# Kernel tuning notes

Measured on AMD Instinct MI355X. Metric: run time of the kernel, lower is better.

## Reference

```python
import jax, jax.numpy as jnp
import numpy as np

HEADS = 4
KNN = 32
N_KEYS = 512
K_DIM = 512
HALF = K_DIM // 2
V_DIM = 1024
IN_DIM = 1024


def setup_inputs() -> dict:
    key = jax.random.key(0)
    k1, k2, k3, k4, k5 = jax.random.split(key, 5)
    x = jax.random.normal(k1, (1, 2048, IN_DIM), dtype=jnp.float32)
    w_q = jax.random.normal(k2, (HEADS * K_DIM, IN_DIM), dtype=jnp.float32) * (IN_DIM ** -0.5)
    b_q = jax.random.normal(k3, (HEADS * K_DIM,), dtype=jnp.float32) * 0.01
    # subkeys: uniform(-1/sqrt(half), 1/sqrt(half)) as in get_uniform_keys
    bound = 1.0 / np.sqrt(HALF)
    keys = jax.random.uniform(k4, (HEADS, 2, N_KEYS, HALF), dtype=jnp.float32,
                              minval=-bound, maxval=bound)
    # values: normal(0, v_dim**-0.5)
    values = jax.random.normal(k5, (N_KEYS * N_KEYS, V_DIM), dtype=jnp.float32) * (V_DIM ** -0.5)
    return {"x": x, "w_q": w_q, "b_q": b_q, "keys": keys, "values": values}


def reference(x, w_q, b_q, keys, values):
    B, S, D = x.shape
    bs = B * S
    # query projection: (bs, heads*k_dim) -> (bs, heads, 2, half)
    q = (x.reshape(bs, D) @ w_q.T + b_q).reshape(bs, HEADS, 2, HALF)
    # per-head, per-half subkey scores: (bs, heads, 2, n_keys)
    scores = jnp.einsum('bhtd,htnd->bhtn', q, keys)
    s_top, i_top = jax.lax.top_k(scores, KNN)          # (bs, heads, 2, knn)
    s1, s2 = s_top[:, :, 0], s_top[:, :, 1]
    i1, i2 = i_top[:, :, 0], i_top[:, :, 1]
    # cross-product of the two half top-k sets: (bs, heads, knn*knn)
    all_s = (s1[..., :, None] + s2[..., None, :]).reshape(bs, HEADS, KNN * KNN)
    all_i = (i1[..., :, None] * N_KEYS + i2[..., None, :]).reshape(bs, HEADS, KNN * KNN)
    best_s, best_pos = jax.lax.top_k(all_s, KNN)       # (bs, heads, knn)
    idx = jnp.take_along_axis(all_i, best_pos, axis=-1)
    # softmax over knn per head (matches softmax on scores.view(-1, knn))
    w = jax.nn.softmax(best_s, axis=-1).reshape(bs, HEADS * KNN)
    idx = idx.reshape(bs, HEADS * KNN)
    # weighted EmbeddingBag gather-sum over the value table
    out = jnp.einsum('bk,bkd->bd', w, values[idx])     # (bs, v_dim)
    return out.reshape(B, S, V_DIM)
```

## Files before the change

### kernel.cpp

```cpp
#include <hip/hip_runtime.h>
#include <math.h>

#define BSZ   2048
#define INDIM 1024
#define QDIM  2048
#define NHT   8
#define NKEYS 512
#define HALFD 256
#define KNN   32
#define VDIM  1024
#define HEADS 4

typedef _Float16 v8h __attribute__((ext_vector_type(8)));
typedef _Float16 v4h __attribute__((ext_vector_type(4)));
typedef float    v4f __attribute__((ext_vector_type(4)));

template<int KSHIFT, bool ASIDE>
__device__ __forceinline__ void split4(const float* __restrict__ in,
                                       _Float16* __restrict__ out, int i) {
  const long e0 = (long)i * 4;
  const int K = 1 << KSHIFT;
  const long r = e0 >> KSHIFT;
  const int k = (int)(e0 & (K - 1));
  const float4 a = *(const float4*)&in[e0];
  const float av[4] = {a.x, a.y, a.z, a.w};
  v4h hv, dv, mv;
  #pragma unroll
  for (int u = 0; u < 4; ++u) {
    const _Float16 hh = (_Float16)av[u];
    hv[u] = hh;
    mv[u] = (_Float16)((av[u] - (float)hh) * 64.0f);
    dv[u] = (_Float16)((float)hh * 0.015625f);
  }
  _Float16* base = out + r * (3L * K) + k;
  *(v4h*)(base)         = hv;
  *(v4h*)(base + K)     = ASIDE ? dv : mv;
  *(v4h*)(base + 2 * K) = ASIDE ? mv : dv;
}

__global__ __launch_bounds__(256) void split_all_kernel(
    const float* __restrict__ x, const float* __restrict__ wq, const float* __restrict__ ky,
    _Float16* __restrict__ xs, _Float16* __restrict__ wqs, _Float16* __restrict__ kys) {
  const int i = blockIdx.x * 256 + threadIdx.x;
  if (i < 524288)            split4<10, true >(x,  xs,  i);
  else if (i < 1048576)      split4<10, false>(wq, wqs, i - 524288);
  else                       split4<8,  false>(ky, kys, i - 1048576);
}

__device__ __forceinline__ void gload16(const _Float16* g, _Float16* l) {
  __builtin_amdgcn_global_load_lds(
      (const __attribute__((address_space(1))) unsigned int*)g,
      (__attribute__((address_space(3))) unsigned int*)l, 16, 0, 0);
}

template<bool Q_EPI>
__global__ __launch_bounds__(256) void mfma_gemm(
    const _Float16* __restrict__ A, int lda, long aBS,
    const _Float16* __restrict__ B, int ldb, long bBS,
    const float* __restrict__ bias,
    float* __restrict__ Cf, int ldc, long cBS,
    _Float16* __restrict__ Cq, int K) {
  extern __shared__ __align__(16) char smem[];
  _Float16* Asm = (_Float16*)smem;
  _Float16* Bsm = (_Float16*)(smem + 16384);
  const int t = threadIdx.x;
  const int z = blockIdx.z;
  const _Float16* Ab = A + (size_t)z * aBS;
  const _Float16* Bb = B + (size_t)z * bBS;
  const int m0 = blockIdx.y * 128, n0 = blockIdx.x * 128;

  const int o0 = t * 16;
  const int os = o0 ^ (((o0 >> 7) & 3) << 4);
  const int sr = os >> 6;
  const int sk = (os & 63) >> 1;
  const _Float16* gA0 = Ab + (size_t)(m0 + sr) * lda + sk;
  const _Float16* gA1 = Ab + (size_t)(m0 + sr + 64) * lda + sk;
  const _Float16* gB0 = Bb + (size_t)(n0 + sr) * ldb + sk;
  const _Float16* gB1 = Bb + (size_t)(n0 + sr + 64) * ldb + sk;

  const int lane = t & 63, w = t >> 6;
  const int wr = (w >> 1) * 64, wc = (w & 1) * 64;
  const int fr = lane & 15, kg = lane >> 4;

  int aoff[4], boff[4];
  #pragma unroll
  for (int i = 0; i < 4; ++i) {
    const int ra = wr + i * 16 + fr;
    aoff[i] = (ra * 64 + ((kg ^ ((ra >> 1) & 3)) * 16)) >> 1;
    const int rb = wc + i * 16 + fr;
    boff[i] = (rb * 64 + ((kg ^ ((rb >> 1) & 3)) * 16)) >> 1;
  }

  v4f acc[4][4];
  #pragma unroll
  for (int i = 0; i < 4; ++i)
    #pragma unroll
    for (int j = 0; j < 4; ++j)
      acc[i][j] = (v4f){0.f, 0.f, 0.f, 0.f};

  gload16(gA0, Asm + t * 8);
  gload16(gA1, Asm + 2048 + t * 8);
  gload16(gB0, Bsm + t * 8);
  gload16(gB1, Bsm + 2048 + t * 8);
  __syncthreads();

  int cur = 0;
  for (int kt = 0; kt < K; kt += 32) {
    const int nxt = cur ^ 1;
    if (kt + 32 < K) {
      gload16(gA0 + kt + 32, Asm + nxt * 4096 + t * 8);
      gload16(gA1 + kt + 32, Asm + nxt * 4096 + 2048 + t * 8);
      gload16(gB0 + kt + 32, Bsm + nxt * 4096 + t * 8);
      gload16(gB1 + kt + 32, Bsm + nxt * 4096 + 2048 + t * 8);
    }
    v8h af[4], bf[4];
    #pragma unroll
    for (int i = 0; i < 4; ++i) af[i] = *(const v8h*)(Asm + cur * 4096 + aoff[i]);
    #pragma unroll
    for (int j = 0; j < 4; ++j) bf[j] = *(const v8h*)(Bsm + cur * 4096 + boff[j]);
    #pragma unroll
    for (int i = 0; i < 4; ++i)
      #pragma unroll
      for (int j = 0; j < 4; ++j)
        acc[i][j] = __builtin_amdgcn_mfma_f32_16x16x32_f16(af[i], bf[j], acc[i][j], 0, 0, 0);
    __syncthreads();
    cur = nxt;
  }

  if (Q_EPI) {
    float* Ct = (float*)smem;
    #pragma unroll
    for (int half = 0; half < 2; ++half) {
      __syncthreads();
      if ((w & 1) == half) {
        #pragma unroll
        for (int j = 0; j < 4; ++j) {
          const int colq = j * 16 + fr;
          const float bv = bias[n0 + half * 64 + colq];
          #pragma unroll
          for (int i = 0; i < 4; ++i)
            #pragma unroll
            for (int rr = 0; rr < 4; ++rr)
              Ct[(wr + i * 16 + kg * 4 + rr) * 68 + colq] = acc[i][j][rr] + bv;
        }
      }
      __syncthreads();
      const int r = t >> 1, cb = (t & 1) * 32;
      const int gcol = n0 + half * 64 + cb;
      const int ht = gcol >> 8, dd = gcol & 255;
      _Float16* p = Cq + (size_t)(m0 + r) * (3 * HALFD * NHT) + ht * (3 * HALFD) + dd;
      #pragma unroll
      for (int u = 0; u < 32; u += 8) {
        float vv[8];
        *(float4*)&vv[0] = *(const float4*)&Ct[r * 68 + cb + u];
        *(float4*)&vv[4] = *(const float4*)&Ct[r * 68 + cb + u + 4];
        v8h hv, dv, mv;
        #pragma unroll
        for (int e = 0; e < 8; ++e) {
          const _Float16 hh = (_Float16)vv[e];
          hv[e] = hh;
          mv[e] = (_Float16)((vv[e] - (float)hh) * 64.0f);
          dv[e] = (_Float16)((float)hh * 0.015625f);
        }
        *(v8h*)(p + u) = hv;
        *(v8h*)(p + HALFD + u) = dv;
        *(v8h*)(p + 2 * HALFD + u) = mv;
      }
    }
  } else {
    float* Cb = Cf + (size_t)z * cBS;
    #pragma unroll
    for (int i = 0; i < 4; ++i)
      #pragma unroll
      for (int j = 0; j < 4; ++j)
        #pragma unroll
        for (int rr = 0; rr < 4; ++rr) {
          const int rowg = m0 + wr + i * 16 + kg * 4 + rr;
          const int colg = n0 + wc + j * 16 + fr;
          Cb[(size_t)rowg * ldc + colg] = acc[i][j][rr];
        }
  }
}

__global__ __launch_bounds__(64) void topk1_kernel(
    const float* __restrict__ S, float* __restrict__ sTop, int* __restrict__ iTop) {
  const int row = blockIdx.x;
  const int lane = threadIdx.x;
  const float* sr = S + (size_t)row * NKEYS;
  float v[8];
  #pragma unroll
  for (int j = 0; j < 8; ++j) v[j] = sr[j * 64 + lane];
  for (int r = 0; r < KNN; ++r) {
    float bv = -INFINITY; int bi = 0x7fffffff;
    #pragma unroll
    for (int j = 0; j < 8; ++j) {
      int idx = j * 64 + lane;
      if (v[j] > bv) { bv = v[j]; bi = idx; }
    }
    #pragma unroll
    for (int off = 32; off > 0; off >>= 1) {
      float ov = __shfl_xor(bv, off);
      int oi = __shfl_xor(bi, off);
      if (ov > bv || (ov == bv && oi < bi)) { bv = ov; bi = oi; }
    }
    if (lane == 0) { sTop[(size_t)row * KNN + r] = bv; iTop[(size_t)row * KNN + r] = bi; }
    const int jj = bi >> 6;
    const bool mine = (bi & 63) == lane;
    #pragma unroll
    for (int j = 0; j < 8; ++j)
      if (mine && j == jj) v[j] = -INFINITY;
  }
}

__global__ __launch_bounds__(256) void topk2_gather_kernel(
    const float* __restrict__ sTop, const int* __restrict__ iTop,
    const float* __restrict__ values, float* __restrict__ out) {
  __shared__ float ls1[4][32], ls2[4][32], sels[4][32];
  __shared__ int   li1[4][32], li2[4][32], seli[4][32];
  __shared__ float lw[128];
  __shared__ int   lidx[128];
  const int b = blockIdx.x, t = threadIdx.x;
  const int lane = t & 63, h = t >> 6;
  const size_t r1 = ((size_t)b * NHT + 2 * h) * KNN;
  if (lane < 32) {
    ls1[h][lane] = sTop[r1 + lane];        li1[h][lane] = iTop[r1 + lane];
    ls2[h][lane] = sTop[r1 + KNN + lane];  li2[h][lane] = iTop[r1 + KNN + lane];
  }
  float v[16];
  #pragma unroll
  for (int c = 0; c < 16; ++c) {
    const int p = c * 64 + lane;
    v[c] = ls1[h][p >> 5] + ls2[h][p & 31];
  }
  for (int r = 0; r < KNN; ++r) {
    float bv = -INFINITY; int bp = 0x7fffffff;
    #pragma unroll
    for (int c = 0; c < 16; ++c) {
      const int p = c * 64 + lane;
      if (v[c] > bv) { bv = v[c]; bp = p; }
    }
    #pragma unroll
    for (int off = 32; off > 0; off >>= 1) {
      const float ov = __shfl_xor(bv, off);
      const int op = __shfl_xor(bp, off);
      if (ov > bv || (ov == bv && op < bp)) { bv = ov; bp = op; }
    }
    if (lane == 0) {
      sels[h][r] = bv;
      seli[h][r] = li1[h][bp >> 5] * NKEYS + li2[h][bp & 31];
    }
    const int cc = bp >> 6;
    const bool mine = (bp & 63) == lane;
    #pragma unroll
    for (int c = 0; c < 16; ++c)
      if (mine && c == cc) v[c] = -INFINITY;
  }
  const float m = sels[h][0];
  const float e = (lane < 32) ? expf(sels[h][lane] - m) : 0.0f;
  float s = e;
  #pragma unroll
  for (int off = 32; off > 0; off >>= 1) s += __shfl_xor(s, off);
  if (lane < 32) {
    lw[h * 32 + lane] = e / s;
    lidx[h * 32 + lane] = seli[h][lane];
  }
  __syncthreads();
  const int d0 = t * 4;
  float4 acc = {0.f, 0.f, 0.f, 0.f};
  #pragma unroll 8
  for (int k = 0; k < 128; ++k) {
    const float4 vv = *(const float4*)&values[(size_t)lidx[k] * VDIM + d0];
    const float ww = lw[k];
    acc.x = fmaf(ww, vv.x, acc.x);
    acc.y = fmaf(ww, vv.y, acc.y);
    acc.z = fmaf(ww, vv.z, acc.z);
    acc.w = fmaf(ww, vv.w, acc.w);
  }
  *(float4*)&out[(size_t)b * VDIM + d0] = acc;
}

extern "C" void kernel_launch(void* const* d_in, const int* in_sizes, int n_in,
                              void* d_out, int out_size, void* d_ws, size_t ws_size,
                              hipStream_t stream) {
  const float* x      = (const float*)d_in[0];
  const float* w_q    = (const float*)d_in[1];
  const float* b_q    = (const float*)d_in[2];
  const float* keys   = (const float*)d_in[3];
  const float* values = (const float*)d_in[4];
  float* out = (float*)d_out;

  char* ws = (char*)d_ws;
  _Float16* xs    = (_Float16*)(ws);
  _Float16* wqs   = (_Float16*)(ws + (16u  << 20));
  _Float16* keyss = (_Float16*)(ws + (32u  << 20));
  _Float16* Qs    = (_Float16*)(ws + (40u  << 20));
  float*    S     = (float*)   (ws + (68u  << 20));
  float*    sTop  = (float*)   (ws + (100u << 20));
  int*      iTop  = (int*)     (ws + (102u << 20));

  split_all_kernel<<<5120, 256, 0, stream>>>(x, w_q, keys, xs, wqs, keyss);

  mfma_gemm<true><<<dim3(QDIM / 128, BSZ / 128, 1), 256, 34816, stream>>>(
      xs, 3 * INDIM, 0, wqs, 3 * INDIM, 0, b_q,
      nullptr, 0, 0, Qs, 3 * INDIM);
  mfma_gemm<false><<<dim3(NKEYS / 128, BSZ / 128, NHT), 256, 32768, stream>>>(
      Qs, 3 * HALFD * NHT, 3 * HALFD, keyss, 3 * HALFD, (long)NKEYS * 3 * HALFD, nullptr,
      S, NHT * NKEYS, NKEYS, nullptr, 3 * HALFD);

  topk1_kernel<<<BSZ * NHT, 64, 0, stream>>>(S, sTop, iTop);
  topk2_gather_kernel<<<BSZ, 256, 0, stream>>>(sTop, iTop, values, out);
}
```

Measured before the change: 377.0 us.

## Deepen GEMM LDS pipeline to four stages with explicit vmcnt waits

Replaces the double-buffered LDS pipeline in the MFMA GEMM with a four-buffer ring that prefetches three K-tiles ahead. A full __syncthreads now becomes a partial s_waitcnt vmcnt followed by a raw barrier, so more global loads stay in flight. The aim is to hide global-to-LDS latency better. In exchange, static LDS grows to 64KB per block, which may lower occupancy. The epilogue also reuses this shared buffer.

```diff
diff --git a/kernel.cpp b/kernel.cpp
--- a/kernel.cpp
+++ b/kernel.cpp
@@ -53,6 +53,10 @@
       (__attribute__((address_space(3))) unsigned int*)l, 16, 0, 0);
 }
 
+#define WAITV8 asm volatile("s_waitcnt vmcnt(8)" ::: "memory")
+#define WAITV4 asm volatile("s_waitcnt vmcnt(4)" ::: "memory")
+#define WAITV0 asm volatile("s_waitcnt vmcnt(0)" ::: "memory")
+
 template<bool Q_EPI>
 __global__ __launch_bounds__(256) void mfma_gemm(
     const _Float16* __restrict__ A, int lda, long aBS,
@@ -60,9 +64,8 @@
     const float* __restrict__ bias,
     float* __restrict__ Cf, int ldc, long cBS,
     _Float16* __restrict__ Cq, int K) {
-  extern __shared__ __align__(16) char smem[];
-  _Float16* Asm = (_Float16*)smem;
-  _Float16* Bsm = (_Float16*)(smem + 16384);
+  __shared__ __align__(16) char smem[65536];
+  _Float16* sh = (_Float16*)smem;
   const int t = threadIdx.x;
   const int z = blockIdx.z;
   const _Float16* Ab = A + (size_t)z * aBS;
@@ -77,6 +80,7 @@
   const _Float16* gA1 = Ab + (size_t)(m0 + sr + 64) * lda + sk;
   const _Float16* gB0 = Bb + (size_t)(n0 + sr) * ldb + sk;
   const _Float16* gB1 = Bb + (size_t)(n0 + sr + 64) * ldb + sk;
+  const int t8 = t * 8;
 
   const int lane = t & 63, w = t >> 6;
   const int wr = (w >> 1) * 64, wc = (w & 1) * 64;
@@ -88,7 +92,7 @@
     const int ra = wr + i * 16 + fr;
     aoff[i] = (ra * 64 + ((kg ^ ((ra >> 1) & 3)) * 16)) >> 1;
     const int rb = wc + i * 16 + fr;
-    boff[i] = (rb * 64 + ((kg ^ ((rb >> 1) & 3)) * 16)) >> 1;
+    boff[i] = ((rb * 64 + ((kg ^ ((rb >> 1) & 3)) * 16)) >> 1) + 4096;
   }
 
   v4f acc[4][4];
@@ -98,33 +102,46 @@
     for (int j = 0; j < 4; ++j)
       acc[i][j] = (v4f){0.f, 0.f, 0.f, 0.f};
 
-  gload16(gA0, Asm + t * 8);
-  gload16(gA1, Asm + 2048 + t * 8);
-  gload16(gB0, Bsm + t * 8);
-  gload16(gB1, Bsm + 2048 + t * 8);
-  __syncthreads();
-
-  int cur = 0;
-  for (int kt = 0; kt < K; kt += 32) {
-    const int nxt = cur ^ 1;
-    if (kt + 32 < K) {
-      gload16(gA0 + kt + 32, Asm + nxt * 4096 + t * 8);
-      gload16(gA1 + kt + 32, Asm + nxt * 4096 + 2048 + t * 8);
-      gload16(gB0 + kt + 32, Bsm + nxt * 4096 + t * 8);
-      gload16(gB1 + kt + 32, Bsm + nxt * 4096 + 2048 + t * 8);
+  const int nt = K >> 5;
+
+  #pragma unroll
+  for (int p = 0; p < 3; ++p) {
+    _Float16* bb = sh + p * 8192;
+    const size_t ko = (size_t)p * 32;
+    gload16(gA0 + ko, bb + t8);
+    gload16(gA1 + ko, bb + 2048 + t8);
+    gload16(gB0 + ko, bb + 4096 + t8);
+    gload16(gB1 + ko, bb + 6144 + t8);
+  }
+  WAITV8;
+  __builtin_amdgcn_s_barrier();
+  __builtin_amdgcn_sched_barrier(0);
+
+  for (int tt = 0; tt < nt; ++tt) {
+    const _Float16* bb = sh + (tt & 3) * 8192;
+    if (tt + 3 < nt) {
+      _Float16* nb = sh + ((tt + 3) & 3) * 8192;
+      const size_t ko = (size_t)(tt + 3) * 32;
+      gload16(gA0 + ko, nb + t8);
+      gload16(gA1 + ko, nb + 2048 + t8);
+      gload16(gB0 + ko, nb + 4096 + t8);
+      gload16(gB1 + ko, nb + 6144 + t8);
     }
     v8h af[4], bf[4];
     #pragma unroll
-    for (int i = 0; i < 4; ++i) af[i] = *(const v8h*)(Asm + cur * 4096 + aoff[i]);
-    #pragma unroll
-    for (int j = 0; j < 4; ++j) bf[j] = *(const v8h*)(Bsm + cur * 4096 + boff[j]);
+    for (int i = 0; i < 4; ++i) af[i] = *(const v8h*)(bb + aoff[i]);
+    #pragma unroll
+    for (int j = 0; j < 4; ++j) bf[j] = *(const v8h*)(bb + boff[j]);
     #pragma unroll
     for (int i = 0; i < 4; ++i)
       #pragma unroll
       for (int j = 0; j < 4; ++j)
         acc[i][j] = __builtin_amdgcn_mfma_f32_16x16x32_f16(af[i], bf[j], acc[i][j], 0, 0, 0);
-    __syncthreads();
-    cur = nxt;
+    if (tt + 3 < nt)      { WAITV8; }
+    else if (tt + 2 < nt) { WAITV4; }
+    else if (tt + 1 < nt) { WAITV0; }
+    __builtin_amdgcn_s_barrier();
+    __builtin_amdgcn_sched_barrier(0);
   }
 
   if (Q_EPI) {
@@ -300,10 +317,10 @@
 
   split_all_kernel<<<5120, 256, 0, stream>>>(x, w_q, keys, xs, wqs, keyss);
 
-  mfma_gemm<true><<<dim3(QDIM / 128, BSZ / 128, 1), 256, 34816, stream>>>(
+  mfma_gemm<true><<<dim3(QDIM / 128, BSZ / 128, 1), 256, 0, stream>>>(
       xs, 3 * INDIM, 0, wqs, 3 * INDIM, 0, b_q,
       nullptr, 0, 0, Qs, 3 * INDIM);
-  mfma_gemm<false><<<dim3(NKEYS / 128, BSZ / 128, NHT), 256, 32768, stream>>>(
+  mfma_gemm<false><<<dim3(NKEYS / 128, BSZ / 128, NHT), 256, 0, stream>>>(
       Qs, 3 * HALFD * NHT, 3 * HALFD, keyss, 3 * HALFD, (long)NKEYS * 3 * HALFD, nullptr,
       S, NHT * NKEYS, NKEYS, nullptr, 3 * HALFD);
 
```

Result: faster. 367.5 us (-2.5%).
